# Kernel tuning notes

Hardware: AMD Instinct MI355X
Metric: run time of the kernel (lower is better)

## Reference

```python
import jax, jax.numpy as jnp
import numpy as np

VOCAB, VDIM, DDIM, BATCH = 50257, 300, 512, 16


def setup_inputs() -> dict:
    key = jax.random.key(0)
    k1, k2, k3, k4, k5 = jax.random.split(key, 5)
    return {
        "decoder_hidden": jax.random.normal(k1, (BATCH, DDIM), dtype=jnp.float32),
        "embedding_vocab": jax.random.normal(k2, (VOCAB, VDIM), dtype=jnp.float32),
        "W_dec": jax.random.normal(k3, (VDIM, DDIM), dtype=jnp.float32) * (1.0 / np.sqrt(DDIM)),
        "b_dec": jax.random.normal(k4, (VDIM,), dtype=jnp.float32) * 0.01,
        "W_full": jax.random.normal(k5, (VDIM,), dtype=jnp.float32) * (1.0 / np.sqrt(VDIM)),
        "b_full": jnp.zeros((), dtype=jnp.float32),
    }


def reference(decoder_hidden, embedding_vocab, W_dec, b_dec, W_full, b_full):
    # query: (B, vocab_dim) = decoder_att(decoder_hidden)
    query = decoder_hidden @ W_dec.T + b_dec
    # additive scores: relu(vocab + query) projected to scalar -> (B, V)
    hidden = jax.nn.relu(embedding_vocab[None, :, :] + query[:, None, :])  # (B, V, D)
    att = jnp.einsum("bvd,d->bv", hidden, W_full) + b_full
    alpha = jax.nn.softmax(att, axis=1)  # softmax over vocab
    # weighted sum of vocab embeddings: (B, vocab_dim)
    attention_weighted_encoding = jnp.einsum("bv,vd->bd", alpha, embedding_vocab)
    return attention_weighted_encoding, alpha
```

## Files before the change

### kernel.cpp

```cpp
#include <hip/hip_runtime.h>

constexpr int V  = 50257;
constexpr int D  = 300;
constexpr int KD = 512;
constexpr int B  = 16;

constexpr int ROWS = 64;
constexpr int NB_ATT = (V + ROWS - 1) / ROWS;
constexpr int NT = 10;
constexpr int NC  = 512;
constexpr int RPC = (V + NC - 1) / NC;

constexpr float NEG_HUGE = -1.0e30f;

constexpr size_t WS_QT   = 0;
constexpr size_t WS_STAT = 4800;
constexpr size_t WS_MS   = WS_STAT + (size_t)NB_ATT * 32;
constexpr size_t WS_PART = WS_MS + 32;
constexpr size_t WS_TMP  = WS_PART + (size_t)NC * 4800;

struct f4 { float v[4]; };
__device__ __forceinline__ f4 ld4(const float* p) {
    float4 t = *(const float4*)p;
    return {t.x, t.y, t.z, t.w};
}

#define AS1 __attribute__((address_space(1)))
#define AS3 __attribute__((address_space(3)))

__global__ void __launch_bounds__(256) k_query(
    const float* __restrict__ dh, const float* __restrict__ Wdec,
    const float* __restrict__ bdec, float* __restrict__ q_t)
{
    int wid  = (blockIdx.x * 256 + threadIdx.x) >> 6;
    int lane = threadIdx.x & 63;
    if (wid >= D * B) return;
    int d = wid >> 4, b = wid & 15;
    const float* wrow = Wdec + (size_t)d * KD;
    const float* hrow = dh + (size_t)b * KD;
    float s = 0.f;
    for (int k = lane; k < KD; k += 64) s += wrow[k] * hrow[k];
    #pragma unroll
    for (int off = 32; off; off >>= 1) s += __shfl_down(s, off, 64);
    if (lane == 0) q_t[d * 16 + b] = s + bdec[d];
}

__global__ void __launch_bounds__(256) k_att(
    const float* __restrict__ E, const float* __restrict__ q_t,
    const float* __restrict__ wf, const float* __restrict__ bf,
    float* __restrict__ att, float* __restrict__ blkstats)
{
    __shared__ float se[3 * 2048];
    __shared__ float sq[5120];
    __shared__ float sw[320];
    __shared__ float smsM[64], smsS[64];

    const int t = threadIdx.x;

    for (int i4 = t * 4; i4 < 5120; i4 += 1024) {
        float4 qv = make_float4(0.f, 0.f, 0.f, 0.f);
        if (i4 < 4800) qv = *(const float4*)(q_t + i4);
        int d = i4 >> 4, bq = (i4 & 15) >> 2;
        int col = (bq + (d >> 2)) & 3;
        *(float4*)(sq + (d << 4) + (col << 2)) = qv;
    }
    for (int i = t; i < 320; i += 256) sw[i] = (i < D) ? wf[i] : 0.f;
    __syncthreads();

    const int v0   = blockIdx.x * ROWS;
    const int slot = t & 7;
    const int s4   = slot << 2;
    const int rloc = t >> 3;
    const int r0   = v0 + rloc;
    const int r1   = r0 + 32;
    const bool va0 = r0 < V, va1 = r1 < V;
    const float* src0 = E + (size_t)(va0 ? r0 : (V - 1)) * D;
    const float* src1 = E + (size_t)(va1 ? r1 : (V - 1)) * D;

    float acc0[16], acc1[16];
    #pragma unroll
    for (int b = 0; b < 16; ++b) { acc0[b] = 0.f; acc1[b] = 0.f; }

#define STAGE(TT, BI) do {                                                    \
    int dd = (TT) * 32 + s4;                                                  \
    if (dd >= D) dd = 0;                                                      \
    float* lb = se + (BI) * 2048 + (t << 2);                                  \
    __builtin_amdgcn_global_load_lds((const AS1 void*)(src0 + dd),            \
                                     (AS3 void*)lb, 16, 0, 0);                \
    __builtin_amdgcn_global_load_lds((const AS1 void*)(src1 + dd),            \
                                     (AS3 void*)(lb + 1024), 16, 0, 0);       \
} while (0)

#define COMPUTE(TT, BI) do {                                                  \
    const float* buf = se + (BI) * 2048;                                      \
    f4 e0 = ld4(buf + (t << 2));                                              \
    f4 e1 = ld4(buf + (t << 2) + 1024);                                       \
    int dbase = (TT) * 32 + s4;                                               \
    _Pragma("unroll")                                                         \
    for (int i = 0; i < 4; ++i) {                                             \
        int d = dbase + i;                                                    \
        float wi = sw[d];                                                     \
        const float* qrow = sq + (d << 4);                                    \
        int rr = d >> 2;                                                      \
        _Pragma("unroll")                                                     \
        for (int bq = 0; bq < 4; ++bq) {                                      \
            f4 qv = ld4(qrow + (((bq + rr) & 3) << 2));                       \
            _Pragma("unroll")                                                 \
            for (int bl = 0; bl < 4; ++bl) {                                  \
                acc0[bq * 4 + bl] = fmaf(fmaxf(e0.v[i] + qv.v[bl], 0.f), wi,  \
                                         acc0[bq * 4 + bl]);                  \
                acc1[bq * 4 + bl] = fmaf(fmaxf(e1.v[i] + qv.v[bl], 0.f), wi,  \
                                         acc1[bq * 4 + bl]);                  \
            }                                                                 \
        }                                                                     \
    }                                                                         \
} while (0)

    STAGE(0, 0);
    STAGE(1, 1);
    for (int tt = 0; tt < NT - 1; ++tt) {
        asm volatile("s_waitcnt vmcnt(2)" ::: "memory");
        __builtin_amdgcn_s_barrier();
        __builtin_amdgcn_sched_barrier(0);
        if (tt < NT - 2) STAGE(tt + 2, (tt + 2) % 3);
        COMPUTE(tt, tt % 3);
    }
    asm volatile("s_waitcnt vmcnt(0)" ::: "memory");
    __builtin_amdgcn_s_barrier();
    __builtin_amdgcn_sched_barrier(0);
    COMPUTE(NT - 1, (NT - 1) % 3);

    #pragma unroll
    for (int b = 0; b < 16; ++b) {
        float x0 = acc0[b], x1 = acc1[b];
        x0 += __shfl_xor(x0, 1, 64); x1 += __shfl_xor(x1, 1, 64);
        x0 += __shfl_xor(x0, 2, 64); x1 += __shfl_xor(x1, 2, 64);
        x0 += __shfl_xor(x0, 4, 64); x1 += __shfl_xor(x1, 4, 64);
        acc0[b] = x0; acc1[b] = x1;
    }

    float bfull = bf[0];
    int b0 = slot * 2;
    float v00 = acc0[b0]     + bfull;
    float v01 = acc0[b0 + 1] + bfull;
    float v10 = acc1[b0]     + bfull;
    float v11 = acc1[b0 + 1] + bfull;
    if (va0) {
        att[(size_t)b0 * V + r0]       = v00;
        att[(size_t)(b0 + 1) * V + r0] = v01;
    }
    if (va1) {
        att[(size_t)b0 * V + r1]       = v10;
        att[(size_t)(b0 + 1) * V + r1] = v11;
    }
    float m0 = fmaxf(va0 ? v00 : NEG_HUGE, va1 ? v10 : NEG_HUGE);
    float m1 = fmaxf(va0 ? v01 : NEG_HUGE, va1 ? v11 : NEG_HUGE);
    float s0 = (va0 ? __expf(v00 - m0) : 0.f) + (va1 ? __expf(v10 - m0) : 0.f);
    float s1 = (va0 ? __expf(v01 - m1) : 0.f) + (va1 ? __expf(v11 - m1) : 0.f);

    #pragma unroll
    for (int mask = 8; mask <= 32; mask <<= 1) {
        float mo = __shfl_xor(m0, mask, 64), so = __shfl_xor(s0, mask, 64);
        float mn = fmaxf(m0, mo);
        s0 = s0 * __expf(m0 - mn) + so * __expf(mo - mn); m0 = mn;
        mo = __shfl_xor(m1, mask, 64); so = __shfl_xor(s1, mask, 64);
        mn = fmaxf(m1, mo);
        s1 = s1 * __expf(m1 - mn) + so * __expf(mo - mn); m1 = mn;
    }
    int wv = t >> 6;
    if ((t & 63) < 8) {
        smsM[wv * 16 + b0] = m0;     smsS[wv * 16 + b0] = s0;
        smsM[wv * 16 + b0 + 1] = m1; smsS[wv * 16 + b0 + 1] = s1;
    }
    __syncthreads();
    if (t < 16) {
        float m = smsM[t], s = smsS[t];
        #pragma unroll
        for (int w = 1; w < 4; ++w) {
            float mo = smsM[w * 16 + t], so = smsS[w * 16 + t];
            float mn = fmaxf(m, mo);
            s = s * __expf(m - mn) + so * __expf(mo - mn);
            m = mn;
        }
        blkstats[((size_t)blockIdx.x * 16 + t) * 2]     = m;
        blkstats[((size_t)blockIdx.x * 16 + t) * 2 + 1] = s;
    }
#undef STAGE
#undef COMPUTE
}

__global__ void __launch_bounds__(64) k_combine(
    const float* __restrict__ blkstats, float* __restrict__ MS)
{
    int b = blockIdx.x, lane = threadIdx.x;
    float m = NEG_HUGE;
    for (int c = lane; c < NB_ATT; c += 64)
        m = fmaxf(m, blkstats[(size_t)(c * 16 + b) * 2]);
    #pragma unroll
    for (int off = 32; off; off >>= 1) m = fmaxf(m, __shfl_xor(m, off, 64));
    float s = 0.f;
    for (int c = lane; c < NB_ATT; c += 64)
        s += blkstats[(size_t)(c * 16 + b) * 2 + 1] *
             __expf(blkstats[(size_t)(c * 16 + b) * 2] - m);
    #pragma unroll
    for (int off = 32; off; off >>= 1) s += __shfl_xor(s, off, 64);
    if (lane == 0) { MS[b * 2] = m; MS[b * 2 + 1] = 1.f / s; }
}

__global__ void __launch_bounds__(320) k_awsum(
    const float* __restrict__ E, float* __restrict__ att,
    const float* __restrict__ MS, float* __restrict__ partials)
{
    __shared__ float sal[RPC * 16];
    int c = blockIdx.x, t = threadIdx.x;
    int v0 = c * RPC;
    int n = V - v0;
    if (n > RPC) n = RPC;
    if (n < 0) n = 0;

    for (int i = t; i < RPC * 16; i += 320) {
        int b = i / RPC, vv = i - b * RPC;
        float a = 0.f;
        if (vv < n) {
            float M = MS[b * 2], invS = MS[b * 2 + 1];
            size_t gi = (size_t)b * V + v0 + vv;
            a = __expf(att[gi] - M) * invS;
            att[gi] = a;
        }
        sal[vv * 16 + b] = a;
    }
    __syncthreads();

    if (t < D) {
        float acc[16];
        #pragma unroll
        for (int b = 0; b < 16; ++b) acc[b] = 0.f;
        #pragma unroll 4
        for (int vv = 0; vv < n; ++vv) {
            float e = E[(size_t)(v0 + vv) * D + t];
            const float* ap = sal + vv * 16;
            f4 a0 = ld4(ap), a1 = ld4(ap + 4), a2 = ld4(ap + 8), a3 = ld4(ap + 12);
            #pragma unroll
            for (int b = 0; b < 4; ++b) {
                acc[b]      = fmaf(a0.v[b], e, acc[b]);
                acc[b + 4]  = fmaf(a1.v[b], e, acc[b + 4]);
                acc[b + 8]  = fmaf(a2.v[b], e, acc[b + 8]);
                acc[b + 12] = fmaf(a3.v[b], e, acc[b + 12]);
            }
        }
        #pragma unroll
        for (int b = 0; b < 16; ++b)
            partials[(size_t)c * 4800 + b * D + t] = acc[b];
    }
}

__global__ void __launch_bounds__(256) k_red1(
    const float* __restrict__ partials, float* __restrict__ tmp)
{
    int o4 = blockIdx.x * 256 + threadIdx.x;
    if (o4 >= 1200) return;
    int y = blockIdx.y;
    float4 s = {0.f, 0.f, 0.f, 0.f};
    for (int c = y * 32; c < y * 32 + 32; ++c) {
        float4 p = *(const float4*)(partials + (size_t)c * 4800 + o4 * 4);
        s.x += p.x; s.y += p.y; s.z += p.z; s.w += p.w;
    }
    *(float4*)(tmp + (size_t)y * 4800 + o4 * 4) = s;
}

__global__ void __launch_bounds__(256) k_red2(
    const float* __restrict__ tmp, float* __restrict__ out)
{
    int o4 = blockIdx.x * 256 + threadIdx.x;
    if (o4 >= 1200) return;
    float4 s = {0.f, 0.f, 0.f, 0.f};
    #pragma unroll
    for (int y = 0; y < 16; ++y) {
        float4 p = *(const float4*)(tmp + (size_t)y * 4800 + o4 * 4);
        s.x += p.x; s.y += p.y; s.z += p.z; s.w += p.w;
    }
    *(float4*)(out + o4 * 4) = s;
}

extern "C" void kernel_launch(void* const* d_in, const int* in_sizes, int n_in,
                              void* d_out, int out_size, void* d_ws, size_t ws_size,
                              hipStream_t stream) {
    const float* dh   = (const float*)d_in[0];
    const float* E    = (const float*)d_in[1];
    const float* Wdec = (const float*)d_in[2];
    const float* bdec = (const float*)d_in[3];
    const float* wf   = (const float*)d_in[4];
    const float* bf   = (const float*)d_in[5];
    float* out = (float*)d_out;
    float* ws  = (float*)d_ws;

    float* q_t   = ws + WS_QT;
    float* stats = ws + WS_STAT;
    float* MS    = ws + WS_MS;
    float* part  = ws + WS_PART;
    float* tmp   = ws + WS_TMP;
    float* att   = out + 4800;

    k_query<<<(D * B + 3) / 4, 256, 0, stream>>>(dh, Wdec, bdec, q_t);
    k_att<<<NB_ATT, 256, 0, stream>>>(E, q_t, wf, bf, att, stats);
    k_combine<<<B, 64, 0, stream>>>(stats, MS);
    k_awsum<<<NC, 320, 0, stream>>>(E, att, MS, part);
    k_red1<<<dim3(5, 16), 256, 0, stream>>>(part, tmp);
    k_red2<<<5, 256, 0, stream>>>(tmp, out);
}
```

Baseline: 82.24 us.

## Restructure attention-score kernel: 4 rows per thread, 64-wide d tiles, DPP reductions

```diff
diff --git a/kernel.cpp b/kernel.cpp
--- a/kernel.cpp
+++ b/kernel.cpp
@@ -7,7 +7,7 @@
 
 constexpr int ROWS = 64;
 constexpr int NB_ATT = (V + ROWS - 1) / ROWS;
-constexpr int NT = 10;
+constexpr int NT = 5;
 constexpr int NC  = 512;
 constexpr int RPC = (V + NC - 1) / NC;
 
@@ -27,6 +27,7 @@
 
 #define AS1 __attribute__((address_space(1)))
 #define AS3 __attribute__((address_space(3)))
+#define DPPF(x, CTRL) __int_as_float(__builtin_amdgcn_mov_dpp(__float_as_int(x), (CTRL), 0xF, 0xF, false))
 
 __global__ void __launch_bounds__(256) k_query(
     const float* __restrict__ dh, const float* __restrict__ Wdec,
@@ -50,67 +51,75 @@
     const float* __restrict__ wf, const float* __restrict__ bf,
     float* __restrict__ att, float* __restrict__ blkstats)
 {
-    __shared__ float se[3 * 2048];
+    __shared__ float se[3 * 4096];
     __shared__ float sq[5120];
     __shared__ float sw[320];
-    __shared__ float smsM[64], smsS[64];
-
-    const int t = threadIdx.x;
-
-    for (int i4 = t * 4; i4 < 5120; i4 += 1024) {
-        float4 qv = make_float4(0.f, 0.f, 0.f, 0.f);
-        if (i4 < 4800) qv = *(const float4*)(q_t + i4);
-        int d = i4 >> 4, bq = (i4 & 15) >> 2;
-        int col = (bq + (d >> 2)) & 3;
-        *(float4*)(sq + (d << 4) + (col << 2)) = qv;
+
+    const int t    = threadIdx.x;
+    const int slot = t & 15;
+    const int rg   = t >> 4;
+    const int s4   = slot << 2;
+    const int v0   = blockIdx.x * ROWS;
+
+    for (int i = t; i < 5120; i += 256) {
+        int d = i >> 4, b = i & 15;
+        int bq = b >> 2, bl = b & 3;
+        float v = (d < D) ? q_t[d * 16 + b] : 0.f;
+        int P = (d >> 1) * 8 + ((((d & 1) << 2) | bq) ^ ((d >> 2) & 7));
+        sq[P * 4 + bl] = v;
     }
     for (int i = t; i < 320; i += 256) sw[i] = (i < D) ? wf[i] : 0.f;
-    __syncthreads();
-
-    const int v0   = blockIdx.x * ROWS;
-    const int slot = t & 7;
-    const int s4   = slot << 2;
-    const int rloc = t >> 3;
-    const int r0   = v0 + rloc;
-    const int r1   = r0 + 32;
-    const bool va0 = r0 < V, va1 = r1 < V;
-    const float* src0 = E + (size_t)(va0 ? r0 : (V - 1)) * D;
-    const float* src1 = E + (size_t)(va1 ? r1 : (V - 1)) * D;
-
-    float acc0[16], acc1[16];
-    #pragma unroll
-    for (int b = 0; b < 16; ++b) { acc0[b] = 0.f; acc1[b] = 0.f; }
+
+    int xq[2][4];
+    #pragma unroll
+    for (int i1 = 0; i1 < 2; ++i1)
+        #pragma unroll
+        for (int bq = 0; bq < 4; ++bq)
+            xq[i1][bq] = slot * 64 + 4 * ((((i1 << 2) | bq)) ^ (slot & 7));
+
+    float acc[4][16];
+    #pragma unroll
+    for (int j = 0; j < 4; ++j)
+        #pragma unroll
+        for (int b = 0; b < 16; ++b) acc[j][b] = 0.f;
+
+    __syncthreads();
 
 #define STAGE(TT, BI) do {                                                    \
-    int dd = (TT) * 32 + s4;                                                  \
-    if (dd >= D) dd = 0;                                                      \
-    float* lb = se + (BI) * 2048 + (t << 2);                                  \
-    __builtin_amdgcn_global_load_lds((const AS1 void*)(src0 + dd),            \
-                                     (AS3 void*)lb, 16, 0, 0);                \
-    __builtin_amdgcn_global_load_lds((const AS1 void*)(src1 + dd),            \
-                                     (AS3 void*)(lb + 1024), 16, 0, 0);       \
+    int dd = (TT) * 64 + s4;                                                  \
+    if (dd >= D) dd = 0;                         \
+    _Pragma("unroll")                                                         \
+    for (int jj = 0; jj < 4; ++jj) {                                          \
+        int row = v0 + jj * 16 + rg;                                          \
+        if (row >= V) row = V - 1;                                            \
+        const float* src = E + (size_t)row * D + dd;                          \
+        float* lb = se + (BI) * 4096 + jj * 1024 + (t << 2);                  \
+        __builtin_amdgcn_global_load_lds((const AS1 void*)src,                \
+                                         (AS3 void*)lb, 16, 0, 0);            \
+    }                                                                         \
 } while (0)
 
 #define COMPUTE(TT, BI) do {                                                  \
-    const float* buf = se + (BI) * 2048;                                      \
-    f4 e0 = ld4(buf + (t << 2));                                              \
-    f4 e1 = ld4(buf + (t << 2) + 1024);                                       \
-    int dbase = (TT) * 32 + s4;                                               \
+    const float* buf = se + (BI) * 4096;                                      \
+    f4 ej[4];                                                                 \
+    _Pragma("unroll")                                                         \
+    for (int j = 0; j < 4; ++j) ej[j] = ld4(buf + rg * 64 + j * 1024 + s4);   \
+    f4 wv = ld4(sw + (TT) * 64 + s4);                                         \
+    const float* sqt = sq + (TT) * 1024;                                      \
     _Pragma("unroll")                                                         \
     for (int i = 0; i < 4; ++i) {                                             \
-        int d = dbase + i;                                                    \
-        float wi = sw[d];                                                     \
-        const float* qrow = sq + (d << 4);                                    \
-        int rr = d >> 2;                                                      \
+        float wi = wv.v[i];                                                   \
         _Pragma("unroll")                                                     \
         for (int bq = 0; bq < 4; ++bq) {                                      \
-            f4 qv = ld4(qrow + (((bq + rr) & 3) << 2));                       \
+            f4 qv = ld4(sqt + (i >> 1) * 32 + xq[i & 1][bq]);                 \
             _Pragma("unroll")                                                 \
-            for (int bl = 0; bl < 4; ++bl) {                                  \
-                acc0[bq * 4 + bl] = fmaf(fmaxf(e0.v[i] + qv.v[bl], 0.f), wi,  \
-                                         acc0[bq * 4 + bl]);                  \
-                acc1[bq * 4 + bl] = fmaf(fmaxf(e1.v[i] + qv.v[bl], 0.f), wi,  \
-                                         acc1[bq * 4 + bl]);                  \
+            for (int j = 0; j < 4; ++j) {                                     \
+                float e = ej[j].v[i];                                         \
+                _Pragma("unroll")                                             \
+                for (int bl = 0; bl < 4; ++bl)                                \
+                    acc[j][bq * 4 + bl] =                                     \
+                        fmaf(fmaxf(e + qv.v[bl], 0.f), wi,                    \
+                             acc[j][bq * 4 + bl]);                            \
             }                                                                 \
         }                                                                     \
     }                                                                         \
@@ -118,75 +127,88 @@
 
     STAGE(0, 0);
     STAGE(1, 1);
-    for (int tt = 0; tt < NT - 1; ++tt) {
-        asm volatile("s_waitcnt vmcnt(2)" ::: "memory");
+    for (int tt = 0; tt < NT; ++tt) {
+        __builtin_amdgcn_sched_barrier(0);
+        if (tt < NT - 1) asm volatile("s_waitcnt vmcnt(4)" ::: "memory");
+        else             asm volatile("s_waitcnt vmcnt(0)" ::: "memory");
         __builtin_amdgcn_s_barrier();
         __builtin_amdgcn_sched_barrier(0);
-        if (tt < NT - 2) STAGE(tt + 2, (tt + 2) % 3);
+        if (tt + 2 < NT) STAGE(tt + 2, (tt + 2) % 3);
         COMPUTE(tt, tt % 3);
     }
-    asm volatile("s_waitcnt vmcnt(0)" ::: "memory");
-    __builtin_amdgcn_s_barrier();
-    __builtin_amdgcn_sched_barrier(0);
-    COMPUTE(NT - 1, (NT - 1) % 3);
-
-    #pragma unroll
-    for (int b = 0; b < 16; ++b) {
-        float x0 = acc0[b], x1 = acc1[b];
-        x0 += __shfl_xor(x0, 1, 64); x1 += __shfl_xor(x1, 1, 64);
-        x0 += __shfl_xor(x0, 2, 64); x1 += __shfl_xor(x1, 2, 64);
-        x0 += __shfl_xor(x0, 4, 64); x1 += __shfl_xor(x1, 4, 64);
-        acc0[b] = x0; acc1[b] = x1;
-    }
-
-    float bfull = bf[0];
-    int b0 = slot * 2;
-    float v00 = acc0[b0]     + bfull;
-    float v01 = acc0[b0 + 1] + bfull;
-    float v10 = acc1[b0]     + bfull;
-    float v11 = acc1[b0 + 1] + bfull;
-    if (va0) {
-        att[(size_t)b0 * V + r0]       = v00;
-        att[(size_t)(b0 + 1) * V + r0] = v01;
-    }
-    if (va1) {
-        att[(size_t)b0 * V + r1]       = v10;
-        att[(size_t)(b0 + 1) * V + r1] = v11;
-    }
-    float m0 = fmaxf(va0 ? v00 : NEG_HUGE, va1 ? v10 : NEG_HUGE);
-    float m1 = fmaxf(va0 ? v01 : NEG_HUGE, va1 ? v11 : NEG_HUGE);
-    float s0 = (va0 ? __expf(v00 - m0) : 0.f) + (va1 ? __expf(v10 - m0) : 0.f);
-    float s1 = (va0 ? __expf(v01 - m1) : 0.f) + (va1 ? __expf(v11 - m1) : 0.f);
-
-    #pragma unroll
-    for (int mask = 8; mask <= 32; mask <<= 1) {
-        float mo = __shfl_xor(m0, mask, 64), so = __shfl_xor(s0, mask, 64);
-        float mn = fmaxf(m0, mo);
-        s0 = s0 * __expf(m0 - mn) + so * __expf(mo - mn); m0 = mn;
-        mo = __shfl_xor(m1, mask, 64); so = __shfl_xor(s1, mask, 64);
-        mn = fmaxf(m1, mo);
-        s1 = s1 * __expf(m1 - mn) + so * __expf(mo - mn); m1 = mn;
-    }
-    int wv = t >> 6;
-    if ((t & 63) < 8) {
-        smsM[wv * 16 + b0] = m0;     smsS[wv * 16 + b0] = s0;
-        smsM[wv * 16 + b0 + 1] = m1; smsS[wv * 16 + b0 + 1] = s1;
+#undef STAGE
+#undef COMPUTE
+
+    #pragma unroll
+    for (int j = 0; j < 4; ++j)
+        #pragma unroll
+        for (int b = 0; b < 16; ++b) {
+            float x = acc[j][b];
+            x += DPPF(x, 0xB1);
+            x += DPPF(x, 0x4E);
+            acc[j][b] = x;
+        }
+    const int c = slot & 3;
+    float kept[4][4];
+    #pragma unroll
+    for (int j = 0; j < 4; ++j)
+        #pragma unroll
+        for (int kk = 0; kk < 4; ++kk) {
+            float x = (c == 0) ? acc[j][kk]
+                    : (c == 1) ? acc[j][4 + kk]
+                    : (c == 2) ? acc[j][8 + kk]
+                    :            acc[j][12 + kk];
+            x += __shfl_xor(x, 4, 64);
+            x += __shfl_xor(x, 8, 64);
+            kept[j][kk] = x;
+        }
+
+    __syncthreads();
+    float* smsM = se;
+    float* smsS = se + 1024;
+
+    const float bfull = bf[0];
+    const int g = (t >> 6) * 16 + (rg & 3) * 4 + (slot >> 2);
+    const int jown = slot >> 2;
+    const int rowown = v0 + rg + 16 * jown;
+    const bool okown = rowown < V;
+
+    #pragma unroll
+    for (int kk = 0; kk < 4; ++kk) {
+        const int b = 4 * c + kk;
+        float x = ((jown == 0) ? kept[0][kk] : (jown == 1) ? kept[1][kk]
+                 : (jown == 2) ? kept[2][kk] : kept[3][kk]) + bfull;
+        if (okown) att[(size_t)b * V + rowown] = x;
+        smsM[g * 16 + b] = okown ? x : NEG_HUGE;
+        smsS[g * 16 + b] = okown ? 1.f : 0.f;
+    }
+    __syncthreads();
+    if (t < 64) {
+        int b = t & 15, q4 = t >> 4;
+        float m = NEG_HUGE, s = 0.f;
+        for (int u = 0; u < 16; ++u) {
+            int gg = q4 * 16 + u;
+            float mg = smsM[gg * 16 + b], sg = smsS[gg * 16 + b];
+            float mn = fmaxf(m, mg);
+            s = s * __expf(m - mn) + sg * __expf(mg - mn);
+            m = mn;
+        }
+        se[2048 + q4 * 16 + b] = m;
+        se[2112 + q4 * 16 + b] = s;
     }
     __syncthreads();
     if (t < 16) {
-        float m = smsM[t], s = smsS[t];
-        #pragma unroll
-        for (int w = 1; w < 4; ++w) {
-            float mo = smsM[w * 16 + t], so = smsS[w * 16 + t];
-            float mn = fmaxf(m, mo);
-            s = s * __expf(m - mn) + so * __expf(mo - mn);
+        float m = NEG_HUGE, s = 0.f;
+        #pragma unroll
+        for (int q4 = 0; q4 < 4; ++q4) {
+            float mg = se[2048 + q4 * 16 + t], sg = se[2112 + q4 * 16 + t];
+            float mn = fmaxf(m, mg);
+            s = s * __expf(m - mn) + sg * __expf(mg - mn);
             m = mn;
         }
         blkstats[((size_t)blockIdx.x * 16 + t) * 2]     = m;
         blkstats[((size_t)blockIdx.x * 16 + t) * 2 + 1] = s;
     }
-#undef STAGE
-#undef COMPUTE
 }
 
 __global__ void __launch_bounds__(64) k_combine(
@@ -194,14 +216,14 @@
 {
     int b = blockIdx.x, lane = threadIdx.x;
     float m = NEG_HUGE;
-    for (int c = lane; c < NB_ATT; c += 64)
-        m = fmaxf(m, blkstats[(size_t)(c * 16 + b) * 2]);
+    for (int cc = lane; cc < NB_ATT; cc += 64)
+        m = fmaxf(m, blkstats[(size_t)(cc * 16 + b) * 2]);
     #pragma unroll
     for (int off = 32; off; off >>= 1) m = fmaxf(m, __shfl_xor(m, off, 64));
     float s = 0.f;
-    for (int c = lane; c < NB_ATT; c += 64)
-        s += blkstats[(size_t)(c * 16 + b) * 2 + 1] *
-             __expf(blkstats[(size_t)(c * 16 + b) * 2] - m);
+    for (int cc = lane; cc < NB_ATT; cc += 64)
+        s += blkstats[(size_t)(cc * 16 + b) * 2 + 1] *
+             __expf(blkstats[(size_t)(cc * 16 + b) * 2] - m);
     #pragma unroll
     for (int off = 32; off; off >>= 1) s += __shfl_xor(s, off, 64);
     if (lane == 0) { MS[b * 2] = m; MS[b * 2 + 1] = 1.f / s; }
```

After: 91.56 us. +11.3%, slower.
